# Kernel tuning notes

Measured on AMD Instinct MI355X. Metric: run time of the kernel, lower is better.

## Reference

```python
import jax, jax.numpy as jnp
import numpy as np

GROUPS = 16
EPS = 1e-6


def conv1x1(x, w, b):
    # x: (B,C,N,K), w: (O,C), b: (O,)
    return jnp.einsum('oc,bcnk->bonk', w, x) + b[None, :, None, None]


def group_norm(x, gamma, beta):
    # GroupNorm(16, C, eps=1e-6, affine=True) over (C/g, N, K) per sample
    B, C, N, K = x.shape
    xg = x.reshape(B, GROUPS, C // GROUPS, N, K)
    mu = xg.mean(axis=(2, 3, 4), keepdims=True)
    var = xg.var(axis=(2, 3, 4), keepdims=True)
    xn = ((xg - mu) * jax.lax.rsqrt(var + EPS)).reshape(B, C, N, K)
    return xn * gamma[None, :, None, None] + beta[None, :, None, None]


def _gather_nbrs(x, idx):
    # x: (B,C,N), idx: (B,N,K) -> (B,C,N,K)
    return jax.vmap(lambda xb, ib: xb[:, ib])(x, idx)


def lse(coords_t, feats, idx, dist, w, b, g, bt):
    # LocalSpatialEncoding: coords_t (B,3,N), feats (B,C,N,1)
    nbr_coords = _gather_nbrs(coords_t, idx)                       # (B,3,N,K)
    ctr_coords = jnp.broadcast_to(coords_t[..., None], nbr_coords.shape)
    concat = jnp.concatenate(
        [ctr_coords, nbr_coords, ctr_coords - nbr_coords, dist[:, None]], axis=1)  # (B,10,N,K)
    enc = jax.nn.relu(group_norm(conv1x1(concat, w, b), g, bt))    # (B,C,N,K)
    nbr_feats = _gather_nbrs(feats[..., 0], idx)                   # (B,C,N,K)
    return jnp.concatenate([enc, nbr_feats], axis=1)               # (B,2C,N,K)


def attentive_pool(x, w, b, g, bt):
    # mean over K, then SharedMLP with GN+ReLU -> (B,O,N,1)
    m = x.mean(axis=-1, keepdims=True)
    return jax.nn.relu(group_norm(conv1x1(m, w, b), g, bt))


def setup_inputs() -> dict:
    B, N, K, D_IN, D_OUT = 2, 32768, 16, 72, 64
    H = D_OUT // 2  # 32
    key = jax.random.key(0)
    ks = jax.random.split(key, 24)

    def w(k, o, i):
        return jax.random.normal(k, (o, i), jnp.float32) * (1.0 / np.sqrt(i))

    inp = {
        'coords': jax.random.normal(ks[0], (B, N, 3), jnp.float32),
        'features': jax.random.normal(ks[1], (B, D_IN, N, 1), jnp.float32),
        'idx': jax.random.randint(ks[2], (B, N, K), 0, N, jnp.int32),
        'dist': jax.random.uniform(ks[3], (B, N, K), jnp.float32),
        # mlp1: d_in -> d_out//2, LeakyReLU(0.2)
        'w_mlp1': w(ks[4], H, D_IN), 'b_mlp1': jnp.zeros((H,), jnp.float32),
        # lse1 mlp: 10 -> H, GN+ReLU
        'w_lse1': w(ks[5], H, 10), 'b_lse1': jnp.zeros((H,), jnp.float32),
        'g_lse1': jnp.ones((H,), jnp.float32), 'bt_lse1': jnp.zeros((H,), jnp.float32),
        # pool1: d_out -> H, GN+ReLU
        'w_pool1': w(ks[6], H, D_OUT), 'b_pool1': jnp.zeros((H,), jnp.float32),
        'g_pool1': jnp.ones((H,), jnp.float32), 'bt_pool1': jnp.zeros((H,), jnp.float32),
        # lse2 mlp: 10 -> H
        'w_lse2': w(ks[7], H, 10), 'b_lse2': jnp.zeros((H,), jnp.float32),
        'g_lse2': jnp.ones((H,), jnp.float32), 'bt_lse2': jnp.zeros((H,), jnp.float32),
        # pool2: d_out -> d_out
        'w_pool2': w(ks[8], D_OUT, D_OUT), 'b_pool2': jnp.zeros((D_OUT,), jnp.float32),
        'g_pool2': jnp.ones((D_OUT,), jnp.float32), 'bt_pool2': jnp.zeros((D_OUT,), jnp.float32),
        # mlp2: d_out -> 2*d_out (no bn, no act)
        'w_mlp2': w(ks[9], 2 * D_OUT, D_OUT), 'b_mlp2': jnp.zeros((2 * D_OUT,), jnp.float32),
        # shortcut: d_in -> 2*d_out, GN, no act
        'w_sc': w(ks[10], 2 * D_OUT, D_IN), 'b_sc': jnp.zeros((2 * D_OUT,), jnp.float32),
        'g_sc': jnp.ones((2 * D_OUT,), jnp.float32), 'bt_sc': jnp.zeros((2 * D_OUT,), jnp.float32),
    }
    return inp


def reference(coords, features, idx, dist,
              w_mlp1, b_mlp1,
              w_lse1, b_lse1, g_lse1, bt_lse1,
              w_pool1, b_pool1, g_pool1, bt_pool1,
              w_lse2, b_lse2, g_lse2, bt_lse2,
              w_pool2, b_pool2, g_pool2, bt_pool2,
              w_mlp2, b_mlp2,
              w_sc, b_sc, g_sc, bt_sc):
    coords_t = coords.transpose(0, 2, 1)                        # (B,3,N)
    x = jax.nn.leaky_relu(conv1x1(features, w_mlp1, b_mlp1), 0.2)   # (B,32,N,1)
    x = lse(coords_t, x, idx, dist, w_lse1, b_lse1, g_lse1, bt_lse1)  # (B,64,N,K)
    x = attentive_pool(x, w_pool1, b_pool1, g_pool1, bt_pool1)        # (B,32,N,1)
    x = lse(coords_t, x, idx, dist, w_lse2, b_lse2, g_lse2, bt_lse2)  # (B,64,N,K)
    x = attentive_pool(x, w_pool2, b_pool2, g_pool2, bt_pool2)        # (B,64,N,1)
    main = conv1x1(x, w_mlp2, b_mlp2)                                 # (B,128,N,1)
    sc = group_norm(conv1x1(features, w_sc, b_sc), g_sc, bt_sc)       # (B,128,N,1)
    return jax.nn.leaky_relu(main + sc, 0.01)
```

## Files before the change

### kernel.cpp

```cpp
#include <hip/hip_runtime.h>

#define NN 32768
#define GEPS 1e-6f

__device__ __forceinline__ float wredsum(float v){
  v += __shfl_xor(v, 32); v += __shfl_xor(v, 16); v += __shfl_xor(v, 8);
  v += __shfl_xor(v, 4);  v += __shfl_xor(v, 2);  v += __shfl_xor(v, 1);
  return v;
}

__global__ void __launch_bounds__(256) f0_prep(
    const float* __restrict__ w_mlp1, const float* __restrict__ b_mlp1,
    const float* __restrict__ w_sc,   const float* __restrict__ b_sc,
    const float* __restrict__ w_pool1,const float* __restrict__ w_pool2,
    float* __restrict__ WallT, float* __restrict__ ball,
    float* __restrict__ wp1T,  float* __restrict__ wp2T)
{
  const int t0 = blockIdx.x*256 + threadIdx.x;
  const int stride = gridDim.x*256;
  for (int u=t0; u<72*160; u+=stride){
    int i = u/160, o = u - i*160;
    WallT[u] = (o < 128) ? w_sc[o*72+i] : w_mlp1[(o-128)*72+i];
  }
  for (int u=t0; u<160; u+=stride)
    ball[u] = (u < 128) ? b_sc[u] : b_mlp1[u-128];
  for (int u=t0; u<64*32; u+=stride){ int c=u>>5, o=u&31; wp1T[u] = w_pool1[o*64+c]; }
  for (int u=t0; u<64*64; u+=stride){ int c=u>>6, o=u&63; wp2T[u] = w_pool2[o*64+c]; }
}

__global__ void __launch_bounds__(256,2) k0_mlp1_scstats(
    const float* __restrict__ feat, const float* __restrict__ WallT,
    const float* __restrict__ ball,
    float* __restrict__ X1, float* __restrict__ scS, float* __restrict__ scQ)
{
  __shared__ float xl[72][128];
  __shared__ float wl[72*32];
  __shared__ float ssl[128], sql[128];
  const int tid = threadIdx.x, lane = tid & 63;
  const int wid = __builtin_amdgcn_readfirstlane(tid >> 6);
  const int b   = __builtin_amdgcn_readfirstlane((int)blockIdx.x >> 8);
  const int n0  = ((int)blockIdx.x & 255) << 7;
  const int p0  = lane*2;

  for (int u=tid; u<72*128; u+=256){
    int c = u>>7, j = u&127;
    xl[c][j] = feat[(size_t)(b*72+c)*NN + n0 + j];
  }

#pragma unroll 1
  for (int pass=0; pass<5; ++pass){
    __syncthreads();
    for (int u=tid; u<2304; u+=256){
      int i = u>>5, c = u&31;
      wl[u] = WallT[i*160 + pass*32 + c];
    }
    __syncthreads();

    const int oc = pass*32 + wid*8;
    float a0[8], a1[8];
#pragma unroll
    for (int q=0;q<8;q++){ float bv = ball[oc+q]; a0[q]=bv; a1[q]=bv; }

    const float* wbase = wl + wid*8;
#pragma unroll
    for (int i=0;i<72;i++){
      const float2 x2 = *(const float2*)&xl[i][p0];
      const float4 w0 = *(const float4*)(wbase + i*32);
      const float4 w1 = *(const float4*)(wbase + i*32 + 4);
      a0[0]=fmaf(w0.x,x2.x,a0[0]); a1[0]=fmaf(w0.x,x2.y,a1[0]);
      a0[1]=fmaf(w0.y,x2.x,a0[1]); a1[1]=fmaf(w0.y,x2.y,a1[1]);
      a0[2]=fmaf(w0.z,x2.x,a0[2]); a1[2]=fmaf(w0.z,x2.y,a1[2]);
      a0[3]=fmaf(w0.w,x2.x,a0[3]); a1[3]=fmaf(w0.w,x2.y,a1[3]);
      a0[4]=fmaf(w1.x,x2.x,a0[4]); a1[4]=fmaf(w1.x,x2.y,a1[4]);
      a0[5]=fmaf(w1.y,x2.x,a0[5]); a1[5]=fmaf(w1.y,x2.y,a1[5]);
      a0[6]=fmaf(w1.z,x2.x,a0[6]); a1[6]=fmaf(w1.z,x2.y,a1[6]);
      a0[7]=fmaf(w1.w,x2.x,a0[7]); a1[7]=fmaf(w1.w,x2.y,a1[7]);
    }

    if (pass < 4){
#pragma unroll
      for (int q=0;q<8;q++){
        float s  = wredsum(a0[q]+a1[q]);
        float s2 = wredsum(a0[q]*a0[q] + a1[q]*a1[q]);
        if (lane==0){ ssl[oc+q] = s; sql[oc+q] = s2; }
      }
    } else {
      __syncthreads();
      float* xst = &xl[0][0];
#pragma unroll
      for (int q=0;q<8;q++){
        float v0 = a0[q], v1 = a1[q];
        v0 = v0 > 0.f ? v0 : 0.2f*v0;
        v1 = v1 > 0.f ? v1 : 0.2f*v1;
        float2 t; t.x=v0; t.y=v1;
        *(float2*)&xst[(wid*8+q)*130 + p0] = t;
      }
      __syncthreads();
      float* xb = X1 + ((size_t)b*NN + n0)*32;
#pragma unroll
      for (int r=0;r<4;r++){
        int u = tid + r*256;
        int p = u>>3, c0 = (u&7)*4;
        float4 o;
        o.x = xst[(c0+0)*130+p]; o.y = xst[(c0+1)*130+p];
        o.z = xst[(c0+2)*130+p]; o.w = xst[(c0+3)*130+p];
        *(float4*)(xb + (size_t)p*32 + c0) = o;
      }
    }
  }

  if (tid < 128){
    atomicAdd(&scS[b*128+tid], ssl[tid]);
    atomicAdd(&scQ[b*128+tid], sql[tid]);
  }
}

__global__ void __launch_bounds__(256) k1_vmom(
    const float* __restrict__ coords, const int* __restrict__ idx,
    const float* __restrict__ dist, float* __restrict__ vm)
{
  __shared__ float red[4*65];
  const int tid = threadIdx.x, lane = tid & 63, wid = tid >> 6;
  const int gn = blockIdx.x*256 + tid;
  const int pt = gn >> 1, h = gn & 1;
  const int b = pt >> 15, n = pt & (NN-1);
  const size_t pb = (size_t)b*NN + n;
  const float c0 = coords[pb*3+0], c1 = coords[pb*3+1], c2 = coords[pb*3+2];

  int ja[8]; float da[8];
  {
    const int4* ip = (const int4*)(idx + pb*16 + h*8);
    const float4* dp = (const float4*)(dist + pb*16 + h*8);
#pragma unroll
    for (int k4=0;k4<2;k4++){
      int4 j4 = ip[k4]; float4 d4 = dp[k4];
      ja[k4*4+0]=j4.x; ja[k4*4+1]=j4.y; ja[k4*4+2]=j4.z; ja[k4*4+3]=j4.w;
      da[k4*4+0]=d4.x; da[k4*4+1]=d4.y; da[k4*4+2]=d4.z; da[k4*4+3]=d4.w;
    }
  }

  float aS[10], aM[55];
#pragma unroll
  for (int i=0;i<10;i++) aS[i]=0.f;
#pragma unroll
  for (int i=0;i<55;i++) aM[i]=0.f;

#pragma unroll
  for (int k=0;k<8;k++){
    const float* nb = coords + ((size_t)b*NN + ja[k])*3;
    const float n0v=nb[0], n1v=nb[1], n2v=nb[2];
    const float v[10] = {c0,c1,c2,n0v,n1v,n2v,c0-n0v,c1-n1v,c2-n2v,da[k]};
#pragma unroll
    for (int i=0;i<10;i++){
      aS[i] += v[i];
#pragma unroll
      for (int j=i;j<10;j++)
        aM[i*10 - (i*(i-1))/2 + (j-i)] += v[i]*v[j];
    }
  }

#pragma unroll
  for (int i=0;i<10;i++){ float s = wredsum(aS[i]); if (lane==0) red[wid*65+i] = s; }
#pragma unroll
  for (int i=0;i<55;i++){ float s = wredsum(aM[i]); if (lane==0) red[wid*65+10+i] = s; }
  __syncthreads();
  if (tid < 65){
    float s = red[tid] + red[65+tid] + red[130+tid] + red[195+tid];
    const int bb = (blockIdx.x*256) >> 16;
    atomicAdd(&vm[bb*65+tid], s);
  }
}

__global__ void f1_fold(
    const float* __restrict__ w_lse1, const float* __restrict__ b_lse1,
    const float* __restrict__ g_lse1, const float* __restrict__ bt_lse1,
    const float* __restrict__ w_lse2, const float* __restrict__ b_lse2,
    const float* __restrict__ g_lse2, const float* __restrict__ bt_lse2,
    const float* __restrict__ vm,
    float* __restrict__ w1p, float* __restrict__ w2p)
{
  const int tid = threadIdx.x;
  const int half = tid >> 6;
  const int u = tid & 63, b = u >> 5, c = u & 31;
  const float* W  = half ? w_lse2  : w_lse1;
  const float* Bv = half ? b_lse2  : b_lse1;
  const float* G  = half ? g_lse2  : g_lse1;
  const float* Bt = half ? bt_lse2 : bt_lse1;
  float wr[10];
#pragma unroll
  for (int i=0;i<10;i++) wr[i] = W[c*10+i];
  const float* S = vm + b*65;
  const float* M = vm + b*65 + 10;
  float P = 0.f;
#pragma unroll
  for (int i=0;i<10;i++) P = fmaf(wr[i], S[i], P);
  float Q = 0.f;
#pragma unroll
  for (int i=0;i<10;i++){
#pragma unroll
    for (int j=i;j<10;j++){
      float m = M[i*10 - (i*(i-1))/2 + (j-i)];
      float t = wr[i]*wr[j]*m;
      Q += (i==j) ? t : 2.f*t;
    }
  }
  const float invNK = 1.f/((float)NN*16.f);
  const float bc = Bv[c];
  float mean = P*invNK + bc;
  float ey2  = (Q + 2.f*bc*P)*invNK + bc*bc;
  float mu = 0.5f*(mean + __shfl_xor(mean,1));
  float e2 = 0.5f*(ey2  + __shfl_xor(ey2, 1));
  float var = e2 - mu*mu;
  float rstd = rsqrtf(var + GEPS);
  float a = G[c]*rstd, d = Bt[c] - mu*a;
  float* out = (half ? w2p : w1p) + (b*32+c)*12;
#pragma unroll
  for (int i=0;i<10;i++) out[i] = wr[i]*a;
  out[10] = bc*a + d;
  out[11] = 0.f;
}

__global__ void __launch_bounds__(128) k2_lse1_pool1(
    const float* __restrict__ coords, const int* __restrict__ idx,
    const float* __restrict__ dist, const float* __restrict__ X1,
    const float* __restrict__ w1p, const float* __restrict__ wp1T,
    const float* __restrict__ b_pool1,
    float* __restrict__ Y1, float* __restrict__ p1S, float* __restrict__ p1Q)
{
  __shared__ float mfl[128*65];
  __shared__ float sl[32], ql[32];
  const int tid = threadIdx.x, lane = tid & 63;
  if (tid < 32){ sl[tid]=0.f; ql[tid]=0.f; }
  __syncthreads();
  const int gn = blockIdx.x*128 + tid;
  const int b = gn >> 15, n = gn & (NN-1);
  const size_t pb = (size_t)b*NN + n;
  float* mf = &mfl[tid*65];

  const float c0=coords[pb*3], c1=coords[pb*3+1], c2=coords[pb*3+2];
  int ja[16]; float da[16]; float nx[16], ny[16], nz[16];
  {
    const int4* ip = (const int4*)(idx + pb*16);
    const float4* dp = (const float4*)(dist + pb*16);
#pragma unroll
    for (int k4=0;k4<4;k4++){
      int4 j4 = ip[k4]; float4 d4 = dp[k4];
      ja[k4*4+0]=j4.x; ja[k4*4+1]=j4.y; ja[k4*4+2]=j4.z; ja[k4*4+3]=j4.w;
      da[k4*4+0]=d4.x; da[k4*4+1]=d4.y; da[k4*4+2]=d4.z; da[k4*4+3]=d4.w;
    }
  }
#pragma unroll
  for (int k=0;k<16;k++){
    const float* nb = coords + ((size_t)b*NN + ja[k])*3;
    nx[k]=nb[0]; ny[k]=nb[1]; nz[k]=nb[2];
  }
  const float s16 = 0.0625f;

#pragma unroll 2
  for (int c=0;c<32;c++){
    const float4* r4 = (const float4*)(w1p + (b*32+c)*12);
    float4 ra=r4[0], rb=r4[1], rc=r4[2];
    const float t0=ra.x+rb.z, t1=ra.y+rb.w, t2=ra.z+rc.x;
    const float u0=ra.w-rb.z, u1=rb.x-rb.w, u2=rb.y-rc.x;
    const float wd=rc.y;
    float cb = rc.z;
    cb = fmaf(t0,c0,cb); cb = fmaf(t1,c1,cb); cb = fmaf(t2,c2,cb);
    float acc = 0.f;
#pragma unroll
    for (int k=0;k<16;k++){
      float s = cb;
      s = fmaf(u0,nx[k],s); s = fmaf(u1,ny[k],s); s = fmaf(u2,nz[k],s);
      s = fmaf(wd,da[k],s);
      acc += fmaxf(s, 0.f);
    }
    mf[c] = acc*s16;
  }

  float4 af[8];
#pragma unroll
  for (int q=0;q<8;q++){ af[q].x=0.f; af[q].y=0.f; af[q].z=0.f; af[q].w=0.f; }
#pragma unroll 2
  for (int k=0;k<16;k++){
    const int j = idx[pb*16+k];
    const float4* g4 = (const float4*)(X1 + ((size_t)b*NN + j)*32);
#pragma unroll
    for (int q=0;q<8;q++){
      float4 g = g4[q];
      af[q].x+=g.x; af[q].y+=g.y; af[q].z+=g.z; af[q].w+=g.w;
    }
  }
#pragma unroll
  for (int q=0;q<8;q++){
    mf[32+q*4+0]=af[q].x*s16; mf[32+q*4+1]=af[q].y*s16;
    mf[32+q*4+2]=af[q].z*s16; mf[32+q*4+3]=af[q].w*s16;
  }

  float yac[32];
#pragma unroll
  for (int o=0;o<32;o++) yac[o] = b_pool1[o];
#pragma unroll 2
  for (int c=0;c<64;c++){
    const float mc = mf[c];
    const float4* col = (const float4*)(wp1T + c*32);
#pragma unroll
    for (int q=0;q<8;q++){
      float4 w = col[q];
      yac[q*4+0] = fmaf(w.x, mc, yac[q*4+0]);
      yac[q*4+1] = fmaf(w.y, mc, yac[q*4+1]);
      yac[q*4+2] = fmaf(w.z, mc, yac[q*4+2]);
      yac[q*4+3] = fmaf(w.w, mc, yac[q*4+3]);
    }
  }
  float4* yo = (float4*)(Y1 + pb*32);
#pragma unroll
  for (int q=0;q<8;q++){
    float4 r; r.x=yac[q*4+0]; r.y=yac[q*4+1]; r.z=yac[q*4+2]; r.w=yac[q*4+3];
    yo[q] = r;
  }
#pragma unroll
  for (int o=0;o<32;o++){
    float s = wredsum(yac[o]);
    float q2 = wredsum(yac[o]*yac[o]);
    if (lane==0){ atomicAdd(&sl[o], s); atomicAdd(&ql[o], q2); }
  }
  __syncthreads();
  if (tid<32){ atomicAdd(&p1S[b*32+tid], sl[tid]); atomicAdd(&p1Q[b*32+tid], ql[tid]); }
}

__global__ void __launch_bounds__(256) f2_apply_pool1(
    float* __restrict__ Y1, const float* __restrict__ p1S, const float* __restrict__ p1Q,
    const float* __restrict__ g, const float* __restrict__ bt)
{
  __shared__ float al[32], dl[32];
  const int tid = threadIdx.x;
  const int b = blockIdx.x >> 10;
  if (tid < 32){
    float s = p1S[b*32+tid], q = p1Q[b*32+tid];
    s += __shfl_xor(s,1); q += __shfl_xor(q,1);
    const float inv = 1.f/(2.f*(float)NN);
    float mu = s*inv, e2 = q*inv, var = e2-mu*mu;
    float rstd = rsqrtf(var + GEPS);
    float a = g[tid]*rstd;
    al[tid] = a; dl[tid] = bt[tid] - mu*a;
  }
  __syncthreads();
  const size_t e4 = (size_t)blockIdx.x*256 + tid;
  float4* Y = (float4*)Y1;
  float4 v = Y[e4];
  const int c0 = ((int)(e4 & 7))*4;
  v.x = fmaxf(fmaf(v.x, al[c0+0], dl[c0+0]), 0.f);
  v.y = fmaxf(fmaf(v.y, al[c0+1], dl[c0+1]), 0.f);
  v.z = fmaxf(fmaf(v.z, al[c0+2], dl[c0+2]), 0.f);
  v.w = fmaxf(fmaf(v.w, al[c0+3], dl[c0+3]), 0.f);
  Y[e4] = v;
}

__global__ void __launch_bounds__(128) k4_lse2_pool2(
    const float* __restrict__ coords, const int* __restrict__ idx,
    const float* __restrict__ dist, const float* __restrict__ Y1,
    const float* __restrict__ w2p, const float* __restrict__ wp2T,
    const float* __restrict__ b_pool2,
    float* __restrict__ Y2T, float* __restrict__ p2S, float* __restrict__ p2Q)
{
  __shared__ float mfl[128*65];
  __shared__ float sl[64], ql[64];
  const int tid = threadIdx.x, lane = tid & 63;
  if (tid < 64){ sl[tid]=0.f; ql[tid]=0.f; }
  __syncthreads();
  const int gn = blockIdx.x*128 + tid;
  const int b = gn >> 15, n = gn & (NN-1);
  const size_t pb = (size_t)b*NN + n;
  float* mf = &mfl[tid*65];

  const float c0=coords[pb*3], c1=coords[pb*3+1], c2=coords[pb*3+2];
  int ja[16]; float da[16]; float nx[16], ny[16], nz[16];
  {
    const int4* ip = (const int4*)(idx + pb*16);
    const float4* dp = (const float4*)(dist + pb*16);
#pragma unroll
    for (int k4=0;k4<4;k4++){
      int4 j4 = ip[k4]; float4 d4 = dp[k4];
      ja[k4*4+0]=j4.x; ja[k4*4+1]=j4.y; ja[k4*4+2]=j4.z; ja[k4*4+3]=j4.w;
      da[k4*4+0]=d4.x; da[k4*4+1]=d4.y; da[k4*4+2]=d4.z; da[k4*4+3]=d4.w;
    }
  }
#pragma unroll
  for (int k=0;k<16;k++){
    const float* nb = coords + ((size_t)b*NN + ja[k])*3;
    nx[k]=nb[0]; ny[k]=nb[1]; nz[k]=nb[2];
  }
  const float s16 = 0.0625f;

#pragma unroll 2
  for (int c=0;c<32;c++){
    const float4* r4 = (const float4*)(w2p + (b*32+c)*12);
    float4 ra=r4[0], rb=r4[1], rc=r4[2];
    const float t0=ra.x+rb.z, t1=ra.y+rb.w, t2=ra.z+rc.x;
    const float u0=ra.w-rb.z, u1=rb.x-rb.w, u2=rb.y-rc.x;
    const float wd=rc.y;
    float cb = rc.z;
    cb = fmaf(t0,c0,cb); cb = fmaf(t1,c1,cb); cb = fmaf(t2,c2,cb);
    float acc = 0.f;
#pragma unroll
    for (int k=0;k<16;k++){
      float s = cb;
      s = fmaf(u0,nx[k],s); s = fmaf(u1,ny[k],s); s = fmaf(u2,nz[k],s);
      s = fmaf(wd,da[k],s);
      acc += fmaxf(s, 0.f);
    }
    mf[c] = acc*s16;
  }

  float4 af[8];
#pragma unroll
  for (int q=0;q<8;q++){ af[q].x=0.f; af[q].y=0.f; af[q].z=0.f; af[q].w=0.f; }
#pragma unroll 2
  for (int k=0;k<16;k++){
    const int j = idx[pb*16+k];
    const float4* g4 = (const float4*)(Y1 + ((size_t)b*NN + j)*32);
#pragma unroll
    for (int q=0;q<8;q++){
      float4 g = g4[q];
      af[q].x+=g.x; af[q].y+=g.y; af[q].z+=g.z; af[q].w+=g.w;
    }
  }
#pragma unroll
  for (int q=0;q<8;q++){
    mf[32+q*4+0]=af[q].x*s16; mf[32+q*4+1]=af[q].y*s16;
    mf[32+q*4+2]=af[q].z*s16; mf[32+q*4+3]=af[q].w*s16;
  }

  float yac[64];
#pragma unroll
  for (int o=0;o<64;o++) yac[o] = b_pool2[o];
#pragma unroll 2
  for (int c=0;c<64;c++){
    const float mc = mf[c];
    const float4* col = (const float4*)(wp2T + c*64);
#pragma unroll
    for (int q=0;q<16;q++){
      float4 w = col[q];
      yac[q*4+0] = fmaf(w.x, mc, yac[q*4+0]);
      yac[q*4+1] = fmaf(w.y, mc, yac[q*4+1]);
      yac[q*4+2] = fmaf(w.z, mc, yac[q*4+2]);
      yac[q*4+3] = fmaf(w.w, mc, yac[q*4+3]);
    }
  }
#pragma unroll
  for (int o=0;o<64;o++)
    Y2T[((size_t)(b*64+o))*NN + n] = yac[o];
#pragma unroll
  for (int o=0;o<64;o++){
    float s = wredsum(yac[o]);
    float q2 = wredsum(yac[o]*yac[o]);
    if (lane==0){ atomicAdd(&sl[o], s); atomicAdd(&ql[o], q2); }
  }
  __syncthreads();
  if (tid<64){ atomicAdd(&p2S[b*64+tid], sl[tid]); atomicAdd(&p2Q[b*64+tid], ql[tid]); }
}

__global__ void f3a_affines(
    const float* __restrict__ scS, const float* __restrict__ scQ,
    const float* __restrict__ g_sc, const float* __restrict__ bt_sc,
    const float* __restrict__ b_sc, const float* __restrict__ b_mlp2,
    const float* __restrict__ p2S, const float* __restrict__ p2Q,
    const float* __restrict__ g_p2, const float* __restrict__ bt_p2,
    float* __restrict__ ascT, float* __restrict__ cstF,
    float* __restrict__ a2F, float* __restrict__ d2F)
{
  const int tid = threadIdx.x;
  if (tid < 256){
    const int b = tid >> 7, c = tid & 127;
    float s = scS[b*128+c], q = scQ[b*128+c];
    s += __shfl_xor(s,1); q += __shfl_xor(q,1);
    s += __shfl_xor(s,2); q += __shfl_xor(q,2);
    s += __shfl_xor(s,4); q += __shfl_xor(q,4);
    const float inv = 1.f/(8.f*(float)NN);
    float mu = s*inv, e2 = q*inv, var = e2-mu*mu;
    float rstd = rsqrtf(var + GEPS);
    float a = g_sc[c]*rstd;
    ascT[tid] = a;
    cstF[tid] = b_mlp2[c] + a*b_sc[c] + (bt_sc[c] - mu*a);
  } else {
    const int t = tid - 256;
    const int b = t >> 6, c = t & 63;
    float s = p2S[b*64+c], q = p2Q[b*64+c];
    s += __shfl_xor(s,1); q += __shfl_xor(q,1);
    s += __shfl_xor(s,2); q += __shfl_xor(q,2);
    const float inv = 1.f/(4.f*(float)NN);
    float mu = s*inv, e2 = q*inv, var = e2-mu*mu;
    float rstd = rsqrtf(var + GEPS);
    float a = g_p2[c]*rstd;
    a2F[t] = a; d2F[t] = bt_p2[c] - mu*a;
  }
}

__global__ void __launch_bounds__(256) f3b_wcomb(
    const float* __restrict__ w_mlp2, const float* __restrict__ w_sc,
    const float* __restrict__ ascT, float* __restrict__ Wcomb)
{
  const int t0 = blockIdx.x*256 + threadIdx.x;
  const int stride = gridDim.x*256;
  for (int u=t0; u<2*136*128; u+=stride){
    int bb = u / 17408;
    int rr = u - bb*17408;
    int i = rr >> 7, o = rr & 127;
    Wcomb[u] = (i < 64) ? w_mlp2[o*64+i]
                        : w_sc[o*72 + (i-64)] * ascT[bb*128+o];
  }
}

__global__ void __launch_bounds__(256,3) k6_final(
    const float* __restrict__ feat, const float* __restrict__ Y2T,
    const float* __restrict__ Wcomb, const float* __restrict__ cstF,
    const float* __restrict__ a2F, const float* __restrict__ d2F,
    float* __restrict__ out)
{
  __shared__ float xl[136][64];
  __shared__ float wl[136*32];
  const int tid = threadIdx.x, lane = tid & 63;
  const int wid = __builtin_amdgcn_readfirstlane(tid >> 6);
  const int b   = __builtin_amdgcn_readfirstlane((int)blockIdx.x >> 9);
  const int n0  = ((int)blockIdx.x & 511) << 6;

  for (int u=tid; u<64*64; u+=256){
    int c = u>>6, j = u&63;
    float y = Y2T[(size_t)(b*64+c)*NN + n0 + j];
    xl[c][j] = fmaxf(fmaf(y, a2F[b*64+c], d2F[b*64+c]), 0.f);
  }
  for (int u=tid; u<72*64; u+=256){
    int c = u>>6, j = u&63;
    xl[64+c][j] = feat[(size_t)(b*72+c)*NN + n0 + j];
  }

  const float* Wb = Wcomb + b*17408;
#pragma unroll 1
  for (int pass=0; pass<4; ++pass){
    __syncthreads();
    for (int u=tid; u<4352; u+=256){
      int i = u>>5, c = u&31;
      wl[u] = Wb[i*128 + pass*32 + c];
    }
    __syncthreads();

    const int oc = pass*32 + wid*8;
    float acc[8];
#pragma unroll
    for (int q=0;q<8;q++) acc[q] = cstF[b*128+oc+q];

    const float* wbase = wl + wid*8;
#pragma unroll
    for (int i=0;i<136;i++){
      const float x = xl[i][lane];
      const float4 w0 = *(const float4*)(wbase + i*32);
      const float4 w1 = *(const float4*)(wbase + i*32 + 4);
      acc[0]=fmaf(w0.x,x,acc[0]); acc[1]=fmaf(w0.y,x,acc[1]);
      acc[2]=fmaf(w0.z,x,acc[2]); acc[3]=fmaf(w0.w,x,acc[3]);
      acc[4]=fmaf(w1.x,x,acc[4]); acc[5]=fmaf(w1.y,x,acc[5]);
      acc[6]=fmaf(w1.z,x,acc[6]); acc[7]=fmaf(w1.w,x,acc[7]);
    }
#pragma unroll
    for (int q=0;q<8;q++){
      float r = acc[q];
      out[((size_t)(b*128+oc+q))*NN + n0 + lane] = r > 0.f ? r : 0.01f*r;
    }
  }
}

extern "C" void kernel_launch(void* const* d_in, const int* in_sizes, int n_in,
                              void* d_out, int out_size, void* d_ws, size_t ws_size,
                              hipStream_t stream) {
  (void)in_sizes; (void)n_in; (void)out_size; (void)ws_size;
  const float* coords  = (const float*)d_in[0];
  const float* feats   = (const float*)d_in[1];
  const int*   idx     = (const int*)  d_in[2];
  const float* dist    = (const float*)d_in[3];
  const float* w_mlp1  = (const float*)d_in[4];
  const float* b_mlp1  = (const float*)d_in[5];
  const float* w_lse1  = (const float*)d_in[6];
  const float* b_lse1  = (const float*)d_in[7];
  const float* g_lse1  = (const float*)d_in[8];
  const float* bt_lse1 = (const float*)d_in[9];
  const float* w_pool1 = (const float*)d_in[10];
  const float* b_pool1 = (const float*)d_in[11];
  const float* g_pool1 = (const float*)d_in[12];
  const float* bt_pool1= (const float*)d_in[13];
  const float* w_lse2  = (const float*)d_in[14];
  const float* b_lse2  = (const float*)d_in[15];
  const float* g_lse2  = (const float*)d_in[16];
  const float* bt_lse2 = (const float*)d_in[17];
  const float* w_pool2 = (const float*)d_in[18];
  const float* b_pool2 = (const float*)d_in[19];
  const float* g_pool2 = (const float*)d_in[20];
  const float* bt_pool2= (const float*)d_in[21];
  const float* w_mlp2  = (const float*)d_in[22];
  const float* b_mlp2  = (const float*)d_in[23];
  const float* w_sc    = (const float*)d_in[24];
  const float* b_sc    = (const float*)d_in[25];
  const float* g_sc    = (const float*)d_in[26];
  const float* bt_sc   = (const float*)d_in[27];

  float* ws   = (float*)d_ws;
  float* scS  = ws;
  float* scQ  = ws + 256;
  float* vm   = ws + 512;
  float* p1S  = ws + 704;
  float* p1Q  = ws + 768;
  float* p2S  = ws + 832;
  float* p2Q  = ws + 960;
  float* w1p  = ws + 1280;
  float* w2p  = ws + 2048;
  float* wp1T = ws + 2816;
  float* wp2T = ws + 4864;
  float* ball = ws + 8960;
  float* cstF = ws + 9120;
  float* a2F  = ws + 9376;
  float* d2F  = ws + 9504;
  float* ascT = ws + 9632;
  float* WallT= ws + 9984;
  float* Wcomb= ws + 21504;
  float* X1   = ws + 57344;
  float* Y1   = X1 + (size_t)2*NN*32;
  float* Y2T  = Y1 + (size_t)2*NN*32;

  hipMemsetAsync(d_ws, 0, 1088*sizeof(float), stream);

  f0_prep<<<32,256,0,stream>>>(w_mlp1,b_mlp1,w_sc,b_sc,w_pool1,w_pool2,
                               WallT,ball,wp1T,wp2T);
  k0_mlp1_scstats<<<512,256,0,stream>>>(feats, WallT, ball, X1, scS, scQ);
  k1_vmom<<<512,256,0,stream>>>(coords, idx, dist, vm);
  f1_fold<<<1,128,0,stream>>>(w_lse1,b_lse1,g_lse1,bt_lse1,
                              w_lse2,b_lse2,g_lse2,bt_lse2,
                              vm, w1p, w2p);
  k2_lse1_pool1<<<512,128,0,stream>>>(coords, idx, dist, X1, w1p, wp1T, b_pool1,
                                      Y1, p1S, p1Q);
  f2_apply_pool1<<<2048,256,0,stream>>>(Y1, p1S, p1Q, g_pool1, bt_pool1);
  k4_lse2_pool2<<<512,128,0,stream>>>(coords, idx, dist, Y1, w2p, wp2T, b_pool2,
                                      Y2T, p2S, p2Q);
  f3a_affines<<<1,384,0,stream>>>(scS,scQ,g_sc,bt_sc,b_sc,b_mlp2,
                                  p2S,p2Q,g_pool2,bt_pool2, ascT,cstF,a2F,d2F);
  f3b_wcomb<<<64,256,0,stream>>>(w_mlp2, w_sc, ascT, Wcomb);
  k6_final<<<1024,256,0,stream>>>(feats, Y2T, Wcomb, cstF, a2F, d2F, (float*)d_out);
}
```

Measured before the change: 278.7 us.

## Split each point across four threads in LSE/pool kernels and moment pass

The moment-accumulation kernel and both LSE+pool kernels now assign four threads per point instead of one (or two). Each thread handles a quarter of the neighbours, channels, or output rows, and the threads share the pooled feature vector through LDS after a block barrier. This raises parallelism and cuts per-thread register arrays (yac[64] becomes yac[16]), which should improve occupancy and memory-level parallelism for the random neighbour gathers. In exchange, the per-point index and coordinate gathers are now duplicated across the four threads, and a barrier is added.

Measured after the change: 390.0 us. +40.0%, slower.

```diff
diff --git a/kernel.cpp b/kernel.cpp
--- a/kernel.cpp
+++ b/kernel.cpp
@@ -6,6 +6,11 @@
 __device__ __forceinline__ float wredsum(float v){
   v += __shfl_xor(v, 32); v += __shfl_xor(v, 16); v += __shfl_xor(v, 8);
   v += __shfl_xor(v, 4);  v += __shfl_xor(v, 2);  v += __shfl_xor(v, 1);
+  return v;
+}
+__device__ __forceinline__ float qredsum(float v){
+  v += __shfl_xor(v, 4); v += __shfl_xor(v, 8);
+  v += __shfl_xor(v, 16); v += __shfl_xor(v, 32);
   return v;
 }
 
@@ -122,21 +127,17 @@
   __shared__ float red[4*65];
   const int tid = threadIdx.x, lane = tid & 63, wid = tid >> 6;
   const int gn = blockIdx.x*256 + tid;
-  const int pt = gn >> 1, h = gn & 1;
+  const int pt = gn >> 2, h = gn & 3;
   const int b = pt >> 15, n = pt & (NN-1);
   const size_t pb = (size_t)b*NN + n;
   const float c0 = coords[pb*3+0], c1 = coords[pb*3+1], c2 = coords[pb*3+2];
 
-  int ja[8]; float da[8];
-  {
-    const int4* ip = (const int4*)(idx + pb*16 + h*8);
-    const float4* dp = (const float4*)(dist + pb*16 + h*8);
-#pragma unroll
-    for (int k4=0;k4<2;k4++){
-      int4 j4 = ip[k4]; float4 d4 = dp[k4];
-      ja[k4*4+0]=j4.x; ja[k4*4+1]=j4.y; ja[k4*4+2]=j4.z; ja[k4*4+3]=j4.w;
-      da[k4*4+0]=d4.x; da[k4*4+1]=d4.y; da[k4*4+2]=d4.z; da[k4*4+3]=d4.w;
-    }
+  int ja[4]; float da[4];
+  {
+    int4 j4 = *(const int4*)(idx + pb*16 + h*4);
+    float4 d4 = *(const float4*)(dist + pb*16 + h*4);
+    ja[0]=j4.x; ja[1]=j4.y; ja[2]=j4.z; ja[3]=j4.w;
+    da[0]=d4.x; da[1]=d4.y; da[2]=d4.z; da[3]=d4.w;
   }
 
   float aS[10], aM[55];
@@ -146,7 +147,7 @@
   for (int i=0;i<55;i++) aM[i]=0.f;
 
 #pragma unroll
-  for (int k=0;k<8;k++){
+  for (int k=0;k<4;k++){
     const float* nb = coords + ((size_t)b*NN + ja[k])*3;
     const float n0v=nb[0], n1v=nb[1], n2v=nb[2];
     const float v[10] = {c0,c1,c2,n0v,n1v,n2v,c0-n0v,c1-n1v,c2-n2v,da[k]};
@@ -166,7 +167,7 @@
   __syncthreads();
   if (tid < 65){
     float s = red[tid] + red[65+tid] + red[130+tid] + red[195+tid];
-    const int bb = (blockIdx.x*256) >> 16;
+    const int bb = blockIdx.x >> 9;
     atomicAdd(&vm[bb*65+tid], s);
   }
 }
@@ -220,45 +221,72 @@
   out[11] = 0.f;
 }
 
-__global__ void __launch_bounds__(128) k2_lse1_pool1(
+__global__ void __launch_bounds__(256,4) k2_lse1_pool1(
     const float* __restrict__ coords, const int* __restrict__ idx,
     const float* __restrict__ dist, const float* __restrict__ X1,
     const float* __restrict__ w1p, const float* __restrict__ wp1T,
     const float* __restrict__ b_pool1,
     float* __restrict__ Y1, float* __restrict__ p1S, float* __restrict__ p1Q)
 {
-  __shared__ float mfl[128*65];
+  __shared__ float mfl[64*65];
   __shared__ float sl[32], ql[32];
   const int tid = threadIdx.x, lane = tid & 63;
+  const int h = tid & 3;
+  const int pl = tid >> 2;
   if (tid < 32){ sl[tid]=0.f; ql[tid]=0.f; }
   __syncthreads();
-  const int gn = blockIdx.x*128 + tid;
-  const int b = gn >> 15, n = gn & (NN-1);
+  const int gpt = blockIdx.x*64 + pl;
+  const int b = gpt >> 15, n = gpt & (NN-1);
   const size_t pb = (size_t)b*NN + n;
-  float* mf = &mfl[tid*65];
-
+  float* mf = &mfl[pl*65];
+  const float s16 = 0.0625f;
+
+  int ja[16];
+  {
+    const int4* ip = (const int4*)(idx + pb*16);
+#pragma unroll
+    for (int k4=0;k4<4;k4++){
+      int4 j4 = ip[k4];
+      ja[k4*4+0]=j4.x; ja[k4*4+1]=j4.y; ja[k4*4+2]=j4.z; ja[k4*4+3]=j4.w;
+    }
+  }
+  {
+    float af0=0,af1=0,af2=0,af3=0,af4=0,af5=0,af6=0,af7=0;
+    const float* xb = X1 + (size_t)b*NN*32 + h*8;
+#pragma unroll 4
+    for (int k=0;k<16;k++){
+      const float4* g4 = (const float4*)(xb + (size_t)ja[k]*32);
+      float4 g0=g4[0], g1=g4[1];
+      af0+=g0.x; af1+=g0.y; af2+=g0.z; af3+=g0.w;
+      af4+=g1.x; af5+=g1.y; af6+=g1.z; af7+=g1.w;
+    }
+    mf[32+h*8+0]=af0*s16; mf[32+h*8+1]=af1*s16;
+    mf[32+h*8+2]=af2*s16; mf[32+h*8+3]=af3*s16;
+    mf[32+h*8+4]=af4*s16; mf[32+h*8+5]=af5*s16;
+    mf[32+h*8+6]=af6*s16; mf[32+h*8+7]=af7*s16;
+  }
+
+  float da[16];
+  {
+    const float4* dp = (const float4*)(dist + pb*16);
+#pragma unroll
+    for (int k4=0;k4<4;k4++){
+      float4 d4 = dp[k4];
+      da[k4*4+0]=d4.x; da[k4*4+1]=d4.y; da[k4*4+2]=d4.z; da[k4*4+3]=d4.w;
+    }
+  }
   const float c0=coords[pb*3], c1=coords[pb*3+1], c2=coords[pb*3+2];
-  int ja[16]; float da[16]; float nx[16], ny[16], nz[16];
-  {
-    const int4* ip = (const int4*)(idx + pb*16);
-    const float4* dp = (const float4*)(dist + pb*16);
-#pragma unroll
-    for (int k4=0;k4<4;k4++){
-      int4 j4 = ip[k4]; float4 d4 = dp[k4];
-      ja[k4*4+0]=j4.x; ja[k4*4+1]=j4.y; ja[k4*4+2]=j4.z; ja[k4*4+3]=j4.w;
-      da[k4*4+0]=d4.x; da[k4*4+1]=d4.y; da[k4*4+2]=d4.z; da[k4*4+3]=d4.w;
-    }
-  }
-#pragma unroll
+  float nx[16], ny[16], nz[16];
+#pragma unroll 4
   for (int k=0;k<16;k++){
     const float* nb = coords + ((size_t)b*NN + ja[k])*3;
     nx[k]=nb[0]; ny[k]=nb[1]; nz[k]=nb[2];
   }
-  const float s16 = 0.0625f;
-
+
+  const float* wrow = w1p + (size_t)(b*32 + h*8)*12;
 #pragma unroll 2
-  for (int c=0;c<32;c++){
-    const float4* r4 = (const float4*)(w1p + (b*32+c)*12);
+  for (int cc=0;cc<8;cc++){
+    const float4* r4 = (const float4*)(wrow + cc*12);
     float4 ra=r4[0], rb=r4[1], rc=r4[2];
     const float t0=ra.x+rb.z, t1=ra.y+rb.w, t2=ra.z+rc.x;
     const float u0=ra.w-rb.z, u1=rb.x-rb.w, u2=rb.y-rc.x;
@@ -273,55 +301,39 @@
       s = fmaf(wd,da[k],s);
       acc += fmaxf(s, 0.f);
     }
-    mf[c] = acc*s16;
-  }
-
-  float4 af[8];
-#pragma unroll
-  for (int q=0;q<8;q++){ af[q].x=0.f; af[q].y=0.f; af[q].z=0.f; af[q].w=0.f; }
-#pragma unroll 2
-  for (int k=0;k<16;k++){
-    const int j = idx[pb*16+k];
-    const float4* g4 = (const float4*)(X1 + ((size_t)b*NN + j)*32);
-#pragma unroll
-    for (int q=0;q<8;q++){
-      float4 g = g4[q];
-      af[q].x+=g.x; af[q].y+=g.y; af[q].z+=g.z; af[q].w+=g.w;
-    }
-  }
-#pragma unroll
-  for (int q=0;q<8;q++){
-    mf[32+q*4+0]=af[q].x*s16; mf[32+q*4+1]=af[q].y*s16;
-    mf[32+q*4+2]=af[q].z*s16; mf[32+q*4+3]=af[q].w*s16;
-  }
-
-  float yac[32];
-#pragma unroll
-  for (int o=0;o<32;o++) yac[o] = b_pool1[o];
-#pragma unroll 2
+    mf[h*8+cc] = acc*s16;
+  }
+  __syncthreads();
+
+  const int o0 = h*8;
+  float yac[8];
+  {
+    const float4 b0 = *(const float4*)(b_pool1 + o0);
+    const float4 b1 = *(const float4*)(b_pool1 + o0 + 4);
+    yac[0]=b0.x; yac[1]=b0.y; yac[2]=b0.z; yac[3]=b0.w;
+    yac[4]=b1.x; yac[5]=b1.y; yac[6]=b1.z; yac[7]=b1.w;
+  }
+#pragma unroll 4
   for (int c=0;c<64;c++){
     const float mc = mf[c];
-    const float4* col = (const float4*)(wp1T + c*32);
-#pragma unroll
-    for (int q=0;q<8;q++){
-      float4 w = col[q];
-      yac[q*4+0] = fmaf(w.x, mc, yac[q*4+0]);
-      yac[q*4+1] = fmaf(w.y, mc, yac[q*4+1]);
-      yac[q*4+2] = fmaf(w.z, mc, yac[q*4+2]);
-      yac[q*4+3] = fmaf(w.w, mc, yac[q*4+3]);
-    }
-  }
-  float4* yo = (float4*)(Y1 + pb*32);
+    const float4 w0 = *(const float4*)(wp1T + c*32 + o0);
+    const float4 w1 = *(const float4*)(wp1T + c*32 + o0 + 4);
+    yac[0]=fmaf(w0.x,mc,yac[0]); yac[1]=fmaf(w0.y,mc,yac[1]);
+    yac[2]=fmaf(w0.z,mc,yac[2]); yac[3]=fmaf(w0.w,mc,yac[3]);
+    yac[4]=fmaf(w1.x,mc,yac[4]); yac[5]=fmaf(w1.y,mc,yac[5]);
+    yac[6]=fmaf(w1.z,mc,yac[6]); yac[7]=fmaf(w1.w,mc,yac[7]);
+  }
+  {
+    float4 r0; r0.x=yac[0]; r0.y=yac[1]; r0.z=yac[2]; r0.w=yac[3];
+    float4 r1; r1.x=yac[4]; r1.y=yac[5]; r1.z=yac[6]; r1.w=yac[7];
+    float* yo = Y1 + pb*32 + o0;
+    ((float4*)yo)[0]=r0; ((float4*)yo)[1]=r1;
+  }
 #pragma unroll
   for (int q=0;q<8;q++){
-    float4 r; r.x=yac[q*4+0]; r.y=yac[q*4+1]; r.z=yac[q*4+2]; r.w=yac[q*4+3];
-    yo[q] = r;
-  }
-#pragma unroll
-  for (int o=0;o<32;o++){
-    float s = wredsum(yac[o]);
-    float q2 = wredsum(yac[o]*yac[o]);
-    if (lane==0){ atomicAdd(&sl[o], s); atomicAdd(&ql[o], q2); }
+    float s  = qredsum(yac[q]);
+    float s2 = qredsum(yac[q]*yac[q]);
+    if (lane < 4){ atomicAdd(&sl[o0+q], s); atomicAdd(&ql[o0+q], s2); }
   }
   __syncthreads();
   if (tid<32){ atomicAdd(&p1S[b*32+tid], sl[tid]); atomicAdd(&p1Q[b*32+tid], ql[tid]); }
@@ -355,45 +367,72 @@
   Y[e4] = v;
 }
 
-__global__ void __launch_bounds__(128) k4_lse2_pool2(
+__global__ void __launch_bounds__(256,4) k4_lse2_pool2(
     const float* __restrict__ coords, const int* __restrict__ idx,
     const float* __restrict__ dist, const float* __restrict__ Y1,
     const float* __restrict__ w2p, const float* __restrict__ wp2T,
     const float* __restrict__ b_pool2,
     float* __restrict__ Y2T, float* __restrict__ p2S, float* __restrict__ p2Q)
 {
-  __shared__ float mfl[128*65];
+  __shared__ float mfl[64*65];
   __shared__ float sl[64], ql[64];
   const int tid = threadIdx.x, lane = tid & 63;
+  const int h = tid & 3;
+  const int pl = tid >> 2;
   if (tid < 64){ sl[tid]=0.f; ql[tid]=0.f; }
   __syncthreads();
-  const int gn = blockIdx.x*128 + tid;
-  const int b = gn >> 15, n = gn & (NN-1);
+  const int gpt = blockIdx.x*64 + pl;
+  const int b = gpt >> 15, n = gpt & (NN-1);
   const size_t pb = (size_t)b*NN + n;
-  float* mf = &mfl[tid*65];
-
+  float* mf = &mfl[pl*65];
+  const float s16 = 0.0625f;
+
+  int ja[16];
+  {
+    const int4* ip = (const int4*)(idx + pb*16);
+#pragma unroll
+    for (int k4=0;k4<4;k4++){
+      int4 j4 = ip[k4];
+      ja[k4*4+0]=j4.x; ja[k4*4+1]=j4.y; ja[k4*4+2]=j4.z; ja[k4*4+3]=j4.w;
+    }
+  }
+  {
+    float af0=0,af1=0,af2=0,af3=0,af4=0,af5=0,af6=0,af7=0;
+    const float* yb = Y1 + (size_t)b*NN*32 + h*8;
+#pragma unroll 4
+    for (int k=0;k<16;k++){
+      const float4* g4 = (const float4*)(yb + (size_t)ja[k]*32);
+      float4 g0=g4[0], g1=g4[1];
+      af0+=g0.x; af1+=g0.y; af2+=g0.z; af3+=g0.w;
+      af4+=g1.x; af5+=g1.y; af6+=g1.z; af7+=g1.w;
+    }
+    mf[32+h*8+0]=af0*s16; mf[32+h*8+1]=af1*s16;
+    mf[32+h*8+2]=af2*s16; mf[32+h*8+3]=af3*s16;
+    mf[32+h*8+4]=af4*s16; mf[32+h*8+5]=af5*s16;
+    mf[32+h*8+6]=af6*s16; mf[32+h*8+7]=af7*s16;
+  }
+
+  float da[16];
+  {
+    const float4* dp = (const float4*)(dist + pb*16);
+#pragma unroll
+    for (int k4=0;k4<4;k4++){
+      float4 d4 = dp[k4];
+      da[k4*4+0]=d4.x; da[k4*4+1]=d4.y; da[k4*4+2]=d4.z; da[k4*4+3]=d4.w;
+    }
+  }
   const float c0=coords[pb*3], c1=coords[pb*3+1], c2=coords[pb*3+2];
-  int ja[16]; float da[16]; float nx[16], ny[16], nz[16];
-  {
-    const int4* ip = (const int4*)(idx + pb*16);
-    const float4* dp = (const float4*)(dist + pb*16);
-#pragma unroll
-    for (int k4=0;k4<4;k4++){
-      int4 j4 = ip[k4]; float4 d4 = dp[k4];
-      ja[k4*4+0]=j4.x; ja[k4*4+1]=j4.y; ja[k4*4+2]=j4.z; ja[k4*4+3]=j4.w;
-      da[k4*4+0]=d4.x; da[k4*4+1]=d4.y; da[k4*4+2]=d4.z; da[k4*4+3]=d4.w;
-    }
-  }
-#pragma unroll
+  float nx[16], ny[16], nz[16];
+#pragma unroll 4
   for (int k=0;k<16;k++){
     const float* nb = coords + ((size_t)b*NN + ja[k])*3;
     nx[k]=nb[0]; ny[k]=nb[1]; nz[k]=nb[2];
   }
-  const float s16 = 0.0625f;
-
+
+  const float* wrow = w2p + (size_t)(b*32 + h*8)*12;
 #pragma unroll 2
-  for (int c=0;c<32;c++){
-    const float4* r4 = (const float4*)(w2p + (b*32+c)*12);
+  for (int cc=0;cc<8;cc++){
+    const float4* r4 = (const float4*)(wrow + cc*12);
     float4 ra=r4[0], rb=r4[1], rc=r4[2];
     const float t0=ra.x+rb.z, t1=ra.y+rb.w, t2=ra.z+rc.x;
     const float u0=ra.w-rb.z, u1=rb.x-rb.w, u2=rb.y-rc.x;
@@ -408,52 +447,42 @@
       s = fmaf(wd,da[k],s);
       acc += fmaxf(s, 0.f);
     }
-    mf[c] = acc*s16;
-  }
-
-  float4 af[8];
-#pragma unroll
-  for (int q=0;q<8;q++){ af[q].x=0.f; af[q].y=0.f; af[q].z=0.f; af[q].w=0.f; }
-#pragma unroll 2
-  for (int k=0;k<16;k++){
-    const int j = idx[pb*16+k];
-    const float4* g4 = (const float4*)(Y1 + ((size_t)b*NN + j)*32);
-#pragma unroll
-    for (int q=0;q<8;q++){
-      float4 g = g4[q];
-      af[q].x+=g.x; af[q].y+=g.y; af[q].z+=g.z; af[q].w+=g.w;
-    }
-  }
-#pragma unroll
-  for (int q=0;q<8;q++){
-    mf[32+q*4+0]=af[q].x*s16; mf[32+q*4+1]=af[q].y*s16;
-    mf[32+q*4+2]=af[q].z*s16; mf[32+q*4+3]=af[q].w*s16;
-  }
-
-  float yac[64];
-#pragma unroll
-  for (int o=0;o<64;o++) yac[o] = b_pool2[o];
-#pragma unroll 2
+    mf[h*8+cc] = acc*s16;
+  }
+  __syncthreads();
+
+  const int o0 = h*16;
+  float yac[16];
+  {
+    const float4* bp = (const float4*)(b_pool2 + o0);
+    float4 b0=bp[0], b1=bp[1], b2=bp[2], b3=bp[3];
+    yac[0]=b0.x; yac[1]=b0.y; yac[2]=b0.z; yac[3]=b0.w;
+    yac[4]=b1.x; yac[5]=b1.y; yac[6]=b1.z; yac[7]=b1.w;
+    yac[8]=b2.x; yac[9]=b2.y; yac[10]=b2.z; yac[11]=b2.w;
+    yac[12]=b3.x; yac[13]=b3.y; yac[14]=b3.z; yac[15]=b3.w;
+  }
+#pragma unroll 4
   for (int c=0;c<64;c++){
     const float mc = mf[c];
-    const float4* col = (const float4*)(wp2T + c*64);
-#pragma unroll
-    for (int q=0;q<16;q++){
-      float4 w = col[q];
-      yac[q*4+0] = fmaf(w.x, mc, yac[q*4+0]);
-      yac[q*4+1] = fmaf(w.y, mc, yac[q*4+1]);
-      yac[q*4+2] = fmaf(w.z, mc, yac[q*4+2]);
-      yac[q*4+3] = fmaf(w.w, mc, yac[q*4+3]);
-    }
-  }
-#pragma unroll
-  for (int o=0;o<64;o++)
-    Y2T[((size_t)(b*64+o))*NN + n] = yac[o];
-#pragma unroll
-  for (int o=0;o<64;o++){
-    float s = wredsum(yac[o]);
-    float q2 = wredsum(yac[o]*yac[o]);
-    if (lane==0){ atomicAdd(&sl[o], s); atomicAdd(&ql[o], q2); }
+    const float4* wr = (const float4*)(wp2T + c*64 + o0);
+    float4 w0=wr[0], w1=wr[1], w2=wr[2], w3=wr[3];
+    yac[0]=fmaf(w0.x,mc,yac[0]); yac[1]=fmaf(w0.y,mc,yac[1]);
+    yac[2]=fmaf(w0.z,mc,yac[2]); yac[3]=fmaf(w0.w,mc,yac[3]);
+    yac[4]=fmaf(w1.x,mc,yac[4]); yac[5]=fmaf(w1.y,mc,yac[5]);
+    yac[6]=fmaf(w1.z,mc,yac[6]); yac[7]=fmaf(w1.w,mc,yac[7]);
+    yac[8]=fmaf(w2.x,mc,yac[8]); yac[9]=fmaf(w2.y,mc,yac[9]);
+    yac[10]=fmaf(w2.z,mc,yac[10]); yac[11]=fmaf(w2.w,mc,yac[11]);
+    yac[12]=fmaf(w3.x,mc,yac[12]); yac[13]=fmaf(w3.y,mc,yac[13]);
+    yac[14]=fmaf(w3.z,mc,yac[14]); yac[15]=fmaf(w3.w,mc,yac[15]);
+  }
+#pragma unroll
+  for (int o=0;o<16;o++)
+    Y2T[((size_t)(b*64+o0+o))*NN + n] = yac[o];
+#pragma unroll
+  for (int q=0;q<16;q++){
+    float s  = qredsum(yac[q]);
+    float s2 = qredsum(yac[q]*yac[q]);
+    if (lane < 4){ atomicAdd(&sl[o0+q], s); atomicAdd(&ql[o0+q], s2); }
   }
   __syncthreads();
   if (tid<64){ atomicAdd(&p2S[b*64+tid], sl[tid]); atomicAdd(&p2Q[b*64+tid], ql[tid]); }
@@ -628,15 +657,15 @@
   f0_prep<<<32,256,0,stream>>>(w_mlp1,b_mlp1,w_sc,b_sc,w_pool1,w_pool2,
                                WallT,ball,wp1T,wp2T);
   k0_mlp1_scstats<<<512,256,0,stream>>>(feats, WallT, ball, X1, scS, scQ);
-  k1_vmom<<<512,256,0,stream>>>(coords, idx, dist, vm);
+  k1_vmom<<<1024,256,0,stream>>>(coords, idx, dist, vm);
   f1_fold<<<1,128,0,stream>>>(w_lse1,b_lse1,g_lse1,bt_lse1,
                               w_lse2,b_lse2,g_lse2,bt_lse2,
                               vm, w1p, w2p);
-  k2_lse1_pool1<<<512,128,0,stream>>>(coords, idx, dist, X1, w1p, wp1T, b_pool1,
-                                      Y1, p1S, p1Q);
+  k2_lse1_pool1<<<1024,256,0,stream>>>(coords, idx, dist, X1, w1p, wp1T, b_pool1,
+                                       Y1, p1S, p1Q);
   f2_apply_pool1<<<2048,256,0,stream>>>(Y1, p1S, p1Q, g_pool1, bt_pool1);
-  k4_lse2_pool2<<<512,128,0,stream>>>(coords, idx, dist, Y1, w2p, wp2T, b_pool2,
-                                      Y2T, p2S, p2Q);
+  k4_lse2_pool2<<<1024,256,0,stream>>>(coords, idx, dist, Y1, w2p, wp2T, b_pool2,
+                                       Y2T, p2S, p2Q);
   f3a_affines<<<1,384,0,stream>>>(scS,scQ,g_sc,bt_sc,b_sc,b_mlp2,
                                   p2S,p2Q,g_pool2,bt_pool2, ascT,cstF,a2F,d2F);
   f3b_wcomb<<<64,256,0,stream>>>(w_mlp2, w_sc, ascT, Wcomb);
```
